# Kernel optimization log

Hardware: AMD Instinct MI355X
Metric: run time of the kernel (lower is better)

The kernel has to match this reference:

```python
import jax, jax.numpy as jnp
from jax import lax
import numpy as np

B, T, NL = 512, 64, 32          # batch, timepoints per patient, n_labs
LAT, HID = 64, 128              # latent_dim, hidden_dim
SCALE, STEP, QPAD, TMAX = 365.0, 0.05, 2000, 2000


def setup_inputs() -> dict:
    key = jax.random.key(0)
    k = jax.random.split(key, 24)
    def rn(ki, shape, s=0.05):
        return jax.random.normal(ki, shape, jnp.float32) * s
    Din = 2 * NL + 1  # GRU input: labs, mask, dt
    return {
        "obs_vals": rn(k[0], (B, T, NL), 1.0),
        "age": jax.random.uniform(k[1], (B,), jnp.float32),
        "eps": rn(k[2], (B, LAT), 1.0),  # reparameterization noise (randn_like)
        "gru_Wih": rn(k[3], (Din, 3 * HID)), "gru_Whh": rn(k[4], (HID, 3 * HID)),
        "gru_bih": jnp.zeros((3 * HID,)), "gru_bhh": jnp.zeros((3 * HID,)),
        "Wmu": rn(k[5], (HID, LAT)), "bmu": jnp.zeros((LAT,)),
        "Wlv": rn(k[6], (HID, LAT)), "blv": jnp.zeros((LAT,)),
        "W1": rn(k[7], (LAT, HID)), "b1": jnp.zeros((HID,)),
        "W2": rn(k[8], (HID, HID)), "b2": jnp.zeros((HID,)),
        "W3": rn(k[9], (HID, LAT)), "b3": jnp.zeros((LAT,)),
        "Wo1": rn(k[10], (LAT, HID)), "bo1": jnp.zeros((HID,)),
        "Wo2": rn(k[11], (HID, NL)), "bo2": jnp.zeros((NL,)),
        "Ws1": rn(k[12], (LAT + 1, HID)), "bs1": jnp.zeros((HID,)),
        "Ws2": rn(k[13], (HID, 2)), "bs2": jnp.zeros((2,)),
        "obs_mask": jax.random.bernoulli(k[14], 0.7, (B, T, NL)),
        "timepoints": jnp.sort(jax.random.randint(k[15], (B, T), 0, TMAX), axis=1).astype(jnp.int32),
        "seq_lens": jax.random.randint(k[16], (B,), 1, T + 1).astype(jnp.int32),
    }


def reference(obs_vals, age, eps, gru_Wih, gru_Whh, gru_bih, gru_bhh,
              Wmu, bmu, Wlv, blv, W1, b1, W2, b2, W3, b3,
              Wo1, bo1, Wo2, bo2, Ws1, bs1, Ws2, bs2,
              obs_mask, timepoints, seq_lens):
    Bv, Tv, Dv = obs_vals.shape
    Hdim = gru_Whh.shape[0]
    tp = timepoints.astype(jnp.float32)

    # ---- RecognitionRNN (GRU over reversed sequence) ----
    dt = jnp.concatenate([jnp.zeros((Bv, 1)), tp[:, 1:] - tp[:, :-1]], axis=1)[..., None]
    maskf = obs_mask.astype(obs_vals.dtype)
    inp = jnp.concatenate([obs_vals * maskf, maskf, dt], axis=-1)  # [B,T,2*NL+1]
    x_seq = jnp.flip(inp, axis=1).transpose(1, 0, 2)  # [T,B,Din]

    def gru_step(h, x):
        gi = x @ gru_Wih + gru_bih
        gh = h @ gru_Whh + gru_bhh
        ir, iz, i_n = jnp.split(gi, 3, axis=-1)
        hr, hz, hn = jnp.split(gh, 3, axis=-1)
        r = jax.nn.sigmoid(ir + hr)
        zg = jax.nn.sigmoid(iz + hz)
        n = jnp.tanh(i_n + r * hn)
        h = (1.0 - zg) * n + zg * h
        return h, None

    h, _ = lax.scan(gru_step, jnp.zeros((Bv, Hdim), obs_vals.dtype), x_seq)
    mu = h @ Wmu + bmu
    logvar = h @ Wlv + blv
    z0 = mu + eps * jnp.exp(0.5 * logvar)  # reparameterize

    # ---- query times (padded unique; timepoints are >= 0 by construction) ----
    qd = jnp.unique(timepoints.reshape(-1), size=QPAD, fill_value=timepoints.max())
    query_t = qd.astype(jnp.float32) / SCALE  # [Q], nondecreasing

    # ---- torchdiffeq fixed-grid rk4 with step_size ----
    qnp = np.asarray(query_t)
    t0, t1 = float(qnp[0]), float(qnp[-1])
    niters = int(np.ceil((t1 - t0) / STEP + 1))
    grid = np.arange(niters) * STEP + t0
    if grid[-1] > t1:
        grid[-1] = t1
    grid = jnp.asarray(grid, jnp.float32)  # [G]

    def ode_f(z):
        return jnp.tanh(jnp.tanh(z @ W1 + b1) @ W2 + b2) @ W3 + b3

    def rk4_step(y, hstep):
        k1 = ode_f(y)
        k2 = ode_f(y + 0.5 * hstep * k1)
        k3 = ode_f(y + 0.5 * hstep * k2)
        k4 = ode_f(y + hstep * k3)
        y2 = y + (hstep / 6.0) * (k1 + 2.0 * k2 + 2.0 * k3 + k4)
        return y2, y2

    _, ys = lax.scan(rk4_step, z0, grid[1:] - grid[:-1])
    ys = jnp.concatenate([z0[None], ys], axis=0)  # [G,B,L]

    # linear interpolation of grid states at query_t (torchdiffeq behavior)
    gi = jnp.clip(jnp.searchsorted(grid, query_t, side="right") - 1, 0, grid.shape[0] - 2)
    tl, tr = grid[gi], grid[gi + 1]
    w = ((query_t - tl) / jnp.where(tr - tl == 0, 1.0, tr - tl))[:, None, None]
    z_traj = ys[gi] * (1.0 - w) + ys[gi + 1] * w  # [Q,B,L]

    # ---- reconstruction loss (vectorized over B,T) ----
    tq = tp / SCALE  # [B,T]
    idx_q = jnp.argmin(jnp.abs(query_t[None, None, :] - tq[:, :, None]), axis=-1)  # [B,T]
    z_bt = z_traj[idx_q, jnp.arange(Bv)[:, None]]  # [B,T,L]
    x_hat = jax.nn.relu(z_bt @ Wo1 + bo1) @ Wo2 + bo2  # [B,T,NL]
    valid = (jnp.arange(Tv)[None, :] < seq_lens[:, None]).astype(obs_vals.dtype)[..., None]
    m = maskf * valid
    n_obs = m.sum()
    recon = jnp.where(n_obs > 0,
                      (m * (x_hat - obs_vals) ** 2).sum() / jnp.maximum(n_obs, 1.0),
                      0.0)

    kl = -0.5 * jnp.mean(jnp.sum(1.0 + logvar - mu ** 2 - jnp.exp(logvar), axis=-1))

    # ---- z_eval at last observed timepoint per patient ----
    last_tp = jnp.take_along_axis(tp, (seq_lens - 1)[:, None], axis=1)[:, 0] / SCALE  # [B]
    idx_e = jnp.argmin(jnp.abs(query_t[None, :] - last_tp[:, None]), axis=-1)  # [B]
    z_eval = z_traj[idx_e, jnp.arange(Bv)]  # [B,L]
    log_hazard = jax.nn.relu(jnp.concatenate([z_eval, age[:, None]], axis=-1) @ Ws1 + bs1) @ Ws2 + bs2
    return log_hazard, recon, kl, z_eval
```

## Files before the change

kernel.cpp:

```cpp
#include <hip/hip_runtime.h>
#include <hip/hip_bf16.h>
#include <math.h>

#define B 512
#define T 64
#define NL 32
#define LAT 64
#define HID 128
#define DIN 65
#define G3 384
#define FSCALE 365.0f
#define MAXGRID 128

#define WS_MIN   0
#define WS_MAX   1
#define WS_NIT   2
#define WS_KL    3
#define WS_RE    4
#define WS_NO    5
#define WS_GRID  8
#define WS_Z0    (WS_GRID + MAXGRID)
#define WS_YS    (WS_Z0 + B*LAT)
#define WS_W31   (WS_YS + 120*B*LAT)
#define WS_B31   (WS_W31 + HID*HID)

typedef __attribute__((ext_vector_type(8))) __bf16 bf16x8;
typedef __attribute__((ext_vector_type(4))) float f32x4;

static __device__ __forceinline__ float tanh_fast(float x){
    float t = __builtin_amdgcn_exp2f(x * 2.8853900817779268f);
    return 1.0f - 2.0f * __builtin_amdgcn_rcpf(t + 1.0f);
}
static __device__ __forceinline__ float sigmoid_fast(float x){
    return __builtin_amdgcn_rcpf(1.0f + __builtin_amdgcn_exp2f(-1.4426950408889634f * x));
}

__global__ void k_init(const int* __restrict__ tp, float* wsf){
    int* wsi = (int*)wsf;
    __shared__ int smin[256], smax[256];
    int tid = threadIdx.x;
    int mn = 2147483647, mx = -2147483647-1;
    for (int i = tid; i < B*T; i += 256){ int v = tp[i]; mn = min(mn,v); mx = max(mx,v); }
    smin[tid]=mn; smax[tid]=mx; __syncthreads();
    for (int s=128; s>0; s>>=1){
        if (tid<s){ smin[tid]=min(smin[tid],smin[tid+s]); smax[tid]=max(smax[tid],smax[tid+s]); }
        __syncthreads();
    }
    if (tid==0){
        wsi[WS_MIN]=smin[0]; wsi[WS_MAX]=smax[0];
        wsf[WS_KL]=0.f; wsf[WS_RE]=0.f; wsf[WS_NO]=0.f;
    }
}

__global__ void k_grid(float* wsf){
    int* wsi=(int*)wsf;
    float t0f = (float)wsi[WS_MIN] / FSCALE;
    float t1f = (float)wsi[WS_MAX] / FSCALE;
    double t0d = (double)t0f, t1d = (double)t1f;
    int nit = (int)ceil((t1d-t0d)/0.05 + 1.0);
    if (nit < 1) nit = 1;
    if (nit > MAXGRID) nit = MAXGRID;
    if (threadIdx.x==0) wsi[WS_NIT] = nit;
    int k = threadIdx.x;
    if (k < nit){
        double g = (double)k * 0.05 + t0d;
        if (k == nit-1 && g > t1d) g = t1d;
        wsf[WS_GRID + k] = (float)g;
    }
}

__global__ __launch_bounds__(256) void k_w31(
    const float* __restrict__ W1, const float* __restrict__ W3,
    const float* __restrict__ b3, float* wsf)
{
    int gid = blockIdx.x*256 + threadIdx.x;
    int k = gid >> 5, n0 = (gid & 31)*4;
    float4 acc = {0.f,0.f,0.f,0.f};
    #pragma unroll 8
    for (int l=0;l<64;++l){
        float w3v = W3[k*LAT + l];
        float4 w1v = *(const float4*)&W1[l*HID + n0];
        acc.x = fmaf(w3v, w1v.x, acc.x);
        acc.y = fmaf(w3v, w1v.y, acc.y);
        acc.z = fmaf(w3v, w1v.z, acc.z);
        acc.w = fmaf(w3v, w1v.w, acc.w);
    }
    *(float4*)&wsf[WS_W31 + k*HID + n0] = acc;
    if (blockIdx.x==0 && threadIdx.x < HID){
        int n = threadIdx.x; float a = 0.f;
        #pragma unroll 8
        for (int l=0;l<64;++l) a = fmaf(b3[l], W1[l*HID+n], a);
        wsf[WS_B31 + n] = a;
    }
}

__global__ __launch_bounds__(512) void k_gru(
    const float* __restrict__ obs, const float* __restrict__ eps,
    const float* __restrict__ Wih, const float* __restrict__ Whh,
    const float* __restrict__ bih, const float* __restrict__ bhh,
    const float* __restrict__ Wmu, const float* __restrict__ bmu,
    const float* __restrict__ Wlv, const float* __restrict__ blv,
    const int* __restrict__ maskI, const int* __restrict__ tp,
    float* wsf)
{
    const int b0 = blockIdx.x * 16;
    const int tid = threadIdx.x;
    const int w = tid >> 6, lane = tid & 63;
    const int g = lane >> 4, c = lane & 15;
    const int xr = tid >> 5, xl = tid & 31;

    __shared__ __align__(16) __bf16 xh[16][232];
    __shared__ int   tps[16][64];
    __shared__ float dts[16];
    __shared__ float lvs[16][64];
    __shared__ float red[8];

    ((int2*)tps)[tid] = ((const int2*)(tp + (size_t)b0*T))[tid];
    {
        unsigned* xz = (unsigned*)&xh[0][0];
        #pragma unroll
        for (int i=0;i<1856;i+=512) xz[i+tid] = 0u;
    }

    bf16x8 wr[6], wz[6], wi[2], wh[4];
    #pragma unroll
    for (int q=0;q<6;++q){
        int kt = q<2 ? q : q+1;
        #pragma unroll
        for (int e=0;e<8;++e){
            int k = kt*32 + g*8 + e;
            float vr, vz;
            if (k < 64){ vr = Wih[k*G3 + 16*w+c];      vz = Wih[k*G3 + 128+16*w+c]; }
            else       { vr = Whh[(k-96)*G3 + 16*w+c]; vz = Whh[(k-96)*G3 + 128+16*w+c]; }
            wr[q][e] = (__bf16)vr; wz[q][e] = (__bf16)vz;
        }
    }
    #pragma unroll
    for (int q=0;q<2;++q)
        #pragma unroll
        for (int e=0;e<8;++e)
            wi[q][e] = (__bf16)Wih[(q*32+g*8+e)*G3 + 256+16*w+c];
    #pragma unroll
    for (int q=0;q<4;++q)
        #pragma unroll
        for (int e=0;e<8;++e)
            wh[q][e] = (__bf16)Whh[(q*32+g*8+e)*G3 + 256+16*w+c];
    const float wdr = Wih[64*G3 + 16*w+c];
    const float wdz = Wih[64*G3 + 128+16*w+c];
    const float wdn = Wih[64*G3 + 256+16*w+c];
    const float rb  = bih[16*w+c]     + bhh[16*w+c];
    const float zb  = bih[128+16*w+c] + bhh[128+16*w+c];
    const float inb = bih[256+16*w+c];
    const float hnb = bhh[256+16*w+c];

    __syncthreads();

    {
        float mv = (float)maskI[((size_t)(b0+xr)*T + 63)*NL + xl];
        float ov = obs[((size_t)(b0+xr)*T + 63)*NL + xl];
        xh[xr][xl]    = (__bf16)(ov*mv);
        xh[xr][32+xl] = (__bf16)mv;
        if (xl==0) dts[xr] = (float)(tps[xr][63]-tps[xr][62]);
    }

    float hold[4] = {0.f,0.f,0.f,0.f};

    for (int s=0;s<T;++s){
        const int t = T-1-s;
        __syncthreads();
        bf16x8 A0 = *(const bf16x8*)&xh[c][0*32 + g*8];
        bf16x8 A1 = *(const bf16x8*)&xh[c][1*32 + g*8];
        bf16x8 A2 = *(const bf16x8*)&xh[c][3*32 + g*8];
        bf16x8 A3 = *(const bf16x8*)&xh[c][4*32 + g*8];
        bf16x8 A4 = *(const bf16x8*)&xh[c][5*32 + g*8];
        bf16x8 A5 = *(const bf16x8*)&xh[c][6*32 + g*8];
        const float dt0=dts[4*g], dt1=dts[4*g+1], dt2=dts[4*g+2], dt3=dts[4*g+3];
        float ov=0.f, mvn=0.f; const int tn = t-1;
        if (s < T-1){
            mvn = (float)maskI[((size_t)(b0+xr)*T + tn)*NL + xl];
            ov  = obs[((size_t)(b0+xr)*T + tn)*NL + xl];
        }
        f32x4 racc={0,0,0,0}, zacc={0,0,0,0}, inacc={0,0,0,0}, hnacc={0,0,0,0};
        racc  = __builtin_amdgcn_mfma_f32_16x16x32_bf16(A0, wr[0], racc, 0,0,0);
        zacc  = __builtin_amdgcn_mfma_f32_16x16x32_bf16(A0, wz[0], zacc, 0,0,0);
        inacc = __builtin_amdgcn_mfma_f32_16x16x32_bf16(A0, wi[0], inacc,0,0,0);
        hnacc = __builtin_amdgcn_mfma_f32_16x16x32_bf16(A2, wh[0], hnacc,0,0,0);
        racc  = __builtin_amdgcn_mfma_f32_16x16x32_bf16(A1, wr[1], racc, 0,0,0);
        zacc  = __builtin_amdgcn_mfma_f32_16x16x32_bf16(A1, wz[1], zacc, 0,0,0);
        inacc = __builtin_amdgcn_mfma_f32_16x16x32_bf16(A1, wi[1], inacc,0,0,0);
        hnacc = __builtin_amdgcn_mfma_f32_16x16x32_bf16(A3, wh[1], hnacc,0,0,0);
        racc  = __builtin_amdgcn_mfma_f32_16x16x32_bf16(A2, wr[2], racc, 0,0,0);
        zacc  = __builtin_amdgcn_mfma_f32_16x16x32_bf16(A2, wz[2], zacc, 0,0,0);
        hnacc = __builtin_amdgcn_mfma_f32_16x16x32_bf16(A4, wh[2], hnacc,0,0,0);
        racc  = __builtin_amdgcn_mfma_f32_16x16x32_bf16(A3, wr[3], racc, 0,0,0);
        zacc  = __builtin_amdgcn_mfma_f32_16x16x32_bf16(A3, wz[3], zacc, 0,0,0);
        hnacc = __builtin_amdgcn_mfma_f32_16x16x32_bf16(A5, wh[3], hnacc,0,0,0);
        racc  = __builtin_amdgcn_mfma_f32_16x16x32_bf16(A4, wr[4], racc, 0,0,0);
        zacc  = __builtin_amdgcn_mfma_f32_16x16x32_bf16(A4, wz[4], zacc, 0,0,0);
        racc  = __builtin_amdgcn_mfma_f32_16x16x32_bf16(A5, wr[5], racc, 0,0,0);
        zacc  = __builtin_amdgcn_mfma_f32_16x16x32_bf16(A5, wz[5], zacc, 0,0,0);
        float hnew[4]; const float dtv[4] = {dt0,dt1,dt2,dt3};
        #pragma unroll
        for (int j=0;j<4;++j){
            float dv = dtv[j];
            float r  = sigmoid_fast(racc[j] + rb + dv*wdr);
            float zg = sigmoid_fast(zacc[j] + zb + dv*wdz);
            float n  = tanh_fast(inacc[j] + inb + dv*wdn + r*(hnacc[j] + hnb));
            float hv = (1.f - zg)*n + zg*hold[j];
            hold[j] = hv; hnew[j] = hv;
        }
        __syncthreads();
        #pragma unroll
        for (int j=0;j<4;++j) xh[4*g+j][96+16*w+c] = (__bf16)hnew[j];
        if (s < T-1){
            xh[xr][xl]    = (__bf16)(ov*mvn);
            xh[xr][32+xl] = (__bf16)mvn;
            if (xl==0) dts[xr] = (tn>0) ? (float)(tps[xr][tn]-tps[xr][tn-1]) : 0.f;
        }
    }
    __syncthreads();

    const int col4 = 16*(w&3)+c;
    bf16x8 Ah0 = *(const bf16x8*)&xh[c][96+0*32+g*8];
    bf16x8 Ah1 = *(const bf16x8*)&xh[c][96+1*32+g*8];
    bf16x8 Ah2 = *(const bf16x8*)&xh[c][96+2*32+g*8];
    bf16x8 Ah3 = *(const bf16x8*)&xh[c][96+3*32+g*8];
    const float* Wm = (w<4)? Wmu : Wlv;
    f32x4 acc={0,0,0,0};
    {
        bf16x8 bf0,bf1,bf2,bf3;
        #pragma unroll
        for (int e=0;e<8;++e){
            bf0[e] = (__bf16)Wm[(0*32+g*8+e)*LAT + col4];
            bf1[e] = (__bf16)Wm[(1*32+g*8+e)*LAT + col4];
            bf2[e] = (__bf16)Wm[(2*32+g*8+e)*LAT + col4];
            bf3[e] = (__bf16)Wm[(3*32+g*8+e)*LAT + col4];
        }
        acc = __builtin_amdgcn_mfma_f32_16x16x32_bf16(Ah0, bf0, acc, 0,0,0);
        acc = __builtin_amdgcn_mfma_f32_16x16x32_bf16(Ah1, bf1, acc, 0,0,0);
        acc = __builtin_amdgcn_mfma_f32_16x16x32_bf16(Ah2, bf2, acc, 0,0,0);
        acc = __builtin_amdgcn_mfma_f32_16x16x32_bf16(Ah3, bf3, acc, 0,0,0);
    }
    const float mbias = (w<4)? bmu[col4] : blv[col4];
    if (w>=4){
        #pragma unroll
        for (int j=0;j<4;++j) lvs[4*g+j][col4] = acc[j] + mbias;
    }
    __syncthreads();
    if (w<4){
        float kl = 0.f;
        #pragma unroll
        for (int j=0;j<4;++j){
            float mu = acc[j] + mbias;
            float lv = lvs[4*g+j][col4];
            int row = b0 + 4*g + j;
            float z0 = mu + eps[(size_t)row*LAT + col4]*expf(0.5f*lv);
            wsf[WS_Z0 + (size_t)row*LAT + col4] = z0;
            wsf[WS_YS + (size_t)row*LAT + col4] = z0;
            kl += 1.f + lv - mu*mu - expf(lv);
        }
        #pragma unroll
        for (int off=32; off>0; off>>=1) kl += __shfl_xor(kl, off);
        if (lane==0) red[w] = kl;
    }
    __syncthreads();
    if (tid==0) atomicAdd(&wsf[WS_KL], red[0]+red[1]+red[2]+red[3]);
}

__global__ __launch_bounds__(256) void k_ode(
    const float* __restrict__ W1, const float* __restrict__ b1,
    const float* __restrict__ W2, const float* __restrict__ b2,
    const float* __restrict__ W3, const float* __restrict__ b3,
    float* wsf)
{
    const int b0 = blockIdx.x * 16;
    const int tid = threadIdx.x;
    const int w = tid >> 6, lane = tid & 63;
    const int g = lane >> 4, c = lane & 15;
    const int lc = 16*w + c;
    const int* wsi = (const int*)wsf;
    const int nit = wsi[WS_NIT];

    __shared__ __align__(16) __bf16 Gl[16][136];
    __shared__ __align__(16) __bf16 Hl[16][136];
    __shared__ float gls[MAXGRID];

    bf16x8 w2f[2][4], w31f[2][4], w3f[4];
    float b1v[2], b2v[2], b31v[2];
    #pragma unroll
    for (int t=0;t<2;++t){
        const int n = 32*w + 16*t + c;
        #pragma unroll
        for (int q=0;q<4;++q)
            #pragma unroll
            for (int e=0;e<8;++e){
                w2f[t][q][e]  = (__bf16)W2[(q*32+g*8+e)*HID + n];
                w31f[t][q][e] = (__bf16)wsf[WS_W31 + (q*32+g*8+e)*HID + n];
            }
        b1v[t]=b1[n]; b2v[t]=b2[n]; b31v[t]=wsf[WS_B31+n];
    }
    #pragma unroll
    for (int q=0;q<4;++q)
        #pragma unroll
        for (int e=0;e<8;++e)
            w3f[q][e] = (__bf16)W3[(q*32+g*8+e)*LAT + lc];
    const float b3v = b3[lc];

    for (int kk=tid; kk<MAXGRID; kk+=256) gls[kk]=wsf[WS_GRID+kk];

    {
        int r = tid>>4, l0 = (tid&15)*4;
        float4 zv = *(const float4*)&wsf[WS_Z0 + (size_t)(b0+r)*LAT + l0];
        Gl[r][l0]   = (__bf16)zv.x; Gl[r][l0+1] = (__bf16)zv.y;
        Gl[r][l0+2] = (__bf16)zv.z; Gl[r][l0+3] = (__bf16)zv.w;
    }
    float y[4];
    #pragma unroll
    for (int j=0;j<4;++j)
        y[j] = wsf[WS_Z0 + (size_t)(b0+4*g+j)*LAT + lc];
    __syncthreads();

    f32x4 U[2];
    {
        bf16x8 az0 = *(const bf16x8*)&Gl[c][g*8];
        bf16x8 az1 = *(const bf16x8*)&Gl[c][32+g*8];
        #pragma unroll
        for (int t=0;t<2;++t){
            const int n = 32*w + 16*t + c;
            bf16x8 wf0, wf1;
            #pragma unroll
            for (int e=0;e<8;++e){
                wf0[e] = (__bf16)W1[(g*8+e)*HID + n];
                wf1[e] = (__bf16)W1[(32+g*8+e)*HID + n];
            }
            f32x4 a = {0.f,0.f,0.f,0.f};
            a = __builtin_amdgcn_mfma_f32_16x16x32_bf16(az0, wf0, a, 0,0,0);
            a = __builtin_amdgcn_mfma_f32_16x16x32_bf16(az1, wf1, a, 0,0,0);
            U[t] = a;
        }
    }
    __syncthreads();

    #pragma unroll
    for (int t=0;t<2;++t)
        #pragma unroll
        for (int j=0;j<4;++j)
            Gl[4*g+j][32*w+16*t+c] = (__bf16)tanh_fast(U[t][j] + b1v[t]);
    __syncthreads();

    f32x4 Uacc0={0,0,0,0}, Uacc1={0,0,0,0}, faccv={0,0,0,0};

    for (int i=0; i<nit-1; ++i){
        const float h = gls[i+1]-gls[i];
        #pragma unroll
        for (int sub=0; sub<4; ++sub){
            {
                bf16x8 a0 = *(const bf16x8*)&Gl[c][g*8];
                bf16x8 a1 = *(const bf16x8*)&Gl[c][32+g*8];
                bf16x8 a2 = *(const bf16x8*)&Gl[c][64+g*8];
                bf16x8 a3 = *(const bf16x8*)&Gl[c][96+g*8];
                #pragma unroll
                for (int t=0;t<2;++t){
                    f32x4 ca={0,0,0,0}, cb={0,0,0,0};
                    ca = __builtin_amdgcn_mfma_f32_16x16x32_bf16(a0, w2f[t][0], ca, 0,0,0);
                    cb = __builtin_amdgcn_mfma_f32_16x16x32_bf16(a2, w2f[t][2], cb, 0,0,0);
                    ca = __builtin_amdgcn_mfma_f32_16x16x32_bf16(a1, w2f[t][1], ca, 0,0,0);
                    cb = __builtin_amdgcn_mfma_f32_16x16x32_bf16(a3, w2f[t][3], cb, 0,0,0);
                    #pragma unroll
                    for (int j=0;j<4;++j)
                        Hl[4*g+j][32*w+16*t+c] = (__bf16)tanh_fast(ca[j]+cb[j]+b2v[t]);
                }
            }
            __syncthreads();
            {
                bf16x8 h0 = *(const bf16x8*)&Hl[c][g*8];
                bf16x8 h1 = *(const bf16x8*)&Hl[c][32+g*8];
                bf16x8 h2 = *(const bf16x8*)&Hl[c][64+g*8];
                bf16x8 h3 = *(const bf16x8*)&Hl[c][96+g*8];
                f32x4 V[2];
                #pragma unroll
                for (int t=0;t<2;++t){
                    f32x4 ca={0,0,0,0}, cb={0,0,0,0};
                    ca = __builtin_amdgcn_mfma_f32_16x16x32_bf16(h0, w31f[t][0], ca, 0,0,0);
                    cb = __builtin_amdgcn_mfma_f32_16x16x32_bf16(h2, w31f[t][2], cb, 0,0,0);
                    ca = __builtin_amdgcn_mfma_f32_16x16x32_bf16(h1, w31f[t][1], ca, 0,0,0);
                    cb = __builtin_amdgcn_mfma_f32_16x16x32_bf16(h3, w31f[t][3], cb, 0,0,0);
                    #pragma unroll
                    for (int j=0;j<4;++j) V[t][j] = ca[j] + cb[j] + b31v[t];
                }
                f32x4 fa={0,0,0,0}, fb={0,0,0,0};
                fa = __builtin_amdgcn_mfma_f32_16x16x32_bf16(h0, w3f[0], fa, 0,0,0);
                fb = __builtin_amdgcn_mfma_f32_16x16x32_bf16(h2, w3f[2], fb, 0,0,0);
                fa = __builtin_amdgcn_mfma_f32_16x16x32_bf16(h1, w3f[1], fa, 0,0,0);
                fb = __builtin_amdgcn_mfma_f32_16x16x32_bf16(h3, w3f[3], fb, 0,0,0);
                if (sub==0){
                    #pragma unroll
                    for (int j=0;j<4;++j) faccv[j] = fa[j]+fb[j]+b3v;
                    Uacc0 = V[0]; Uacc1 = V[1];
                } else if (sub==3){
                    #pragma unroll
                    for (int j=0;j<4;++j) faccv[j] += fa[j]+fb[j]+b3v;
                    Uacc0 += V[0]; Uacc1 += V[1];
                } else {
                    #pragma unroll
                    for (int j=0;j<4;++j) faccv[j] += 2.f*(fa[j]+fb[j]+b3v);
                    Uacc0 += 2.f*V[0]; Uacc1 += 2.f*V[1];
                }
                if (sub < 3){
                    const float al = (sub==2) ? h : 0.5f*h;
                    #pragma unroll
                    for (int t=0;t<2;++t)
                        #pragma unroll
                        for (int j=0;j<4;++j)
                            Gl[4*g+j][32*w+16*t+c] =
                                (__bf16)tanh_fast(U[t][j] + al*V[t][j] + b1v[t]);
                } else {
                    const float h6 = h*(1.0f/6.0f);
                    #pragma unroll
                    for (int j=0;j<4;++j){
                        y[j] = fmaf(h6, faccv[j], y[j]);
                        wsf[WS_YS + ((size_t)(i+1)*B + (b0+4*g+j))*LAT + lc] = y[j];
                    }
                    U[0] += h6*Uacc0; U[1] += h6*Uacc1;
                    #pragma unroll
                    for (int t=0;t<2;++t)
                        #pragma unroll
                        for (int j=0;j<4;++j)
                            Gl[4*g+j][32*w+16*t+c] = (__bf16)tanh_fast(U[t][j] + b1v[t]);
                }
            }
            __syncthreads();
        }
    }
}

__global__ __launch_bounds__(512) void k_recon(
    const float* __restrict__ obs, const int* __restrict__ maskI,
    const int* __restrict__ tp, const int* __restrict__ seq,
    const float* __restrict__ Wo1, const float* __restrict__ bo1,
    const float* __restrict__ Wo2, const float* __restrict__ bo2,
    float* wsf)
{
    const int b = blockIdx.x, tid = threadIdx.x;
    const int w = tid >> 6, lane = tid & 63;
    const int g = lane >> 4, c = lane & 15;
    __shared__ __align__(16) __bf16 zbt[64][72];
    __shared__ __align__(16) __bf16 hb[64][136];
    __shared__ float gls[MAXGRID];
    __shared__ float red[16];
    const int* wsi=(const int*)wsf;
    const int nit = wsi[WS_NIT];
    for (int i=tid;i<MAXGRID;i+=512) gls[i]=wsf[WS_GRID+i];

    bf16x8 wo1f[2], wo2f[4];
    #pragma unroll
    for (int q=0;q<2;++q)
        #pragma unroll
        for (int e=0;e<8;++e)
            wo1f[q][e] = (__bf16)Wo1[(q*32+g*8+e)*HID + 16*w+c];
    {
        int n = w & 1;
        #pragma unroll
        for (int q=0;q<4;++q)
            #pragma unroll
            for (int e=0;e<8;++e)
                wo2f[q][e] = (__bf16)Wo2[(q*32+g*8+e)*NL + 16*n+c];
    }
    const float bo1v = bo1[16*w+c];
    const float bo2v = bo2[16*(w&1)+c];
    const int sl = seq[b];
    __syncthreads();

    {
        int t = tid >> 3, seg = tid & 7;
        float tq = (float)tp[b*T+t] / FSCALE;
        int lo=0, hi=nit;
        while (lo<hi){ int mid=(lo+hi)>>1; if (gls[mid]<=tq) lo=mid+1; else hi=mid; }
        int k = lo-1; if (k<0) k=0; if (nit>=2 && k>nit-2) k=nit-2; if (nit<2) k=0;
        float wq=0.f;
        if (nit>=2){ float tl=gls[k], tr=gls[k+1]; float den=(tr-tl==0.f)?1.f:(tr-tl); wq=(tq-tl)/den; }
        size_t o0 = (size_t)WS_YS + ((size_t)k*B + b)*LAT + seg*8;
        float4 za0 = *(const float4*)&wsf[o0];
        float4 za1 = *(const float4*)&wsf[o0+4];
        float4 zb0, zb1;
        if (nit>=2){
            zb0 = *(const float4*)&wsf[o0 + (size_t)B*LAT];
            zb1 = *(const float4*)&wsf[o0 + (size_t)B*LAT + 4];
        } else { zb0 = za0; zb1 = za1; }
        __bf16* dst = &zbt[t][seg*8];
        dst[0] = (__bf16)(za0.x*(1.f-wq)+zb0.x*wq);
        dst[1] = (__bf16)(za0.y*(1.f-wq)+zb0.y*wq);
        dst[2] = (__bf16)(za0.z*(1.f-wq)+zb0.z*wq);
        dst[3] = (__bf16)(za0.w*(1.f-wq)+zb0.w*wq);
        dst[4] = (__bf16)(za1.x*(1.f-wq)+zb1.x*wq);
        dst[5] = (__bf16)(za1.y*(1.f-wq)+zb1.y*wq);
        dst[6] = (__bf16)(za1.z*(1.f-wq)+zb1.z*wq);
        dst[7] = (__bf16)(za1.w*(1.f-wq)+zb1.w*wq);
    }
    __syncthreads();

    #pragma unroll
    for (int m=0;m<4;++m){
        f32x4 acc = {0.f,0.f,0.f,0.f};
        bf16x8 a0 = *(const bf16x8*)&zbt[16*m+c][g*8];
        bf16x8 a1 = *(const bf16x8*)&zbt[16*m+c][32+g*8];
        acc = __builtin_amdgcn_mfma_f32_16x16x32_bf16(a0, wo1f[0], acc, 0,0,0);
        acc = __builtin_amdgcn_mfma_f32_16x16x32_bf16(a1, wo1f[1], acc, 0,0,0);
        #pragma unroll
        for (int j=0;j<4;++j)
            hb[16*m+4*g+j][16*w+c] = (__bf16)fmaxf(acc[j] + bo1v, 0.f);
    }
    __syncthreads();

    float esum = 0.f, ncnt = 0.f;
    {
        int m = w >> 1, n = w & 1;
        f32x4 ca = {0.f,0.f,0.f,0.f}, cb = {0.f,0.f,0.f,0.f};
        bf16x8 a0 = *(const bf16x8*)&hb[16*m+c][g*8];
        bf16x8 a1 = *(const bf16x8*)&hb[16*m+c][32+g*8];
        bf16x8 a2 = *(const bf16x8*)&hb[16*m+c][64+g*8];
        bf16x8 a3 = *(const bf16x8*)&hb[16*m+c][96+g*8];
        ca = __builtin_amdgcn_mfma_f32_16x16x32_bf16(a0, wo2f[0], ca, 0,0,0);
        cb = __builtin_amdgcn_mfma_f32_16x16x32_bf16(a2, wo2f[2], cb, 0,0,0);
        ca = __builtin_amdgcn_mfma_f32_16x16x32_bf16(a1, wo2f[1], ca, 0,0,0);
        cb = __builtin_amdgcn_mfma_f32_16x16x32_bf16(a3, wo2f[3], cb, 0,0,0);
        #pragma unroll
        for (int j=0;j<4;++j){
            int t = 16*m + 4*g + j;
            int col = 16*n + c;
            float xh2 = (ca[j]+cb[j]) + bo2v;
            float mv = (float)maskI[(b*T+t)*NL+col] * ((t<sl)?1.f:0.f);
            float d = xh2 - obs[(b*T+t)*NL+col];
            esum = fmaf(mv*d, d, esum);
            ncnt += mv;
        }
    }
    #pragma unroll
    for (int off=32; off>0; off>>=1){
        esum += __shfl_xor(esum, off);
        ncnt += __shfl_xor(ncnt, off);
    }
    if (lane==0){ red[w] = esum; red[8+w] = ncnt; }
    __syncthreads();
    if (tid==0){
        float s=0.f, nn=0.f;
        #pragma unroll
        for (int i=0;i<8;++i){ s += red[i]; nn += red[8+i]; }
        atomicAdd(&wsf[WS_RE], s);
        atomicAdd(&wsf[WS_NO], nn);
    }
}

__global__ __launch_bounds__(128) void k_surv(
    const float* __restrict__ age, const int* __restrict__ tp, const int* __restrict__ seq,
    const float* __restrict__ Ws1, const float* __restrict__ bs1,
    const float* __restrict__ Ws2, const float* __restrict__ bs2,
    float* wsf, float* out)
{
    int b=blockIdx.x, tid=threadIdx.x;
    __shared__ float gls[MAXGRID];
    __shared__ float ze[64];
    __shared__ float pred[4];
    const int* wsi=(const int*)wsf; int nit=wsi[WS_NIT];
    for (int i=tid;i<MAXGRID;i+=128) gls[i]=wsf[WS_GRID+i];
    __syncthreads();
    int sl = seq[b];
    float tq = (float)tp[b*T + sl-1] / FSCALE;
    int lo=0,hi=nit;
    while(lo<hi){int mid=(lo+hi)>>1; if (gls[mid]<=tq) lo=mid+1; else hi=mid;}
    int k=lo-1; if(k<0)k=0; if(nit>=2 && k>nit-2)k=nit-2; if (nit<2) k=0;
    float w=0.f;
    if (nit>=2){ float tl=gls[k],tr=gls[k+1]; float den=(tr-tl==0.f)?1.f:(tr-tl); w=(tq-tl)/den; }
    if (tid<LAT){
        size_t o0 = (size_t)WS_YS + ((size_t)k*B+b)*LAT+tid;
        float zl = wsf[o0]*(1.f-w) + ((nit>=2)? wsf[o0+(size_t)B*LAT]*w : 0.f);
        ze[tid]=zl;
        out[1026 + b*LAT + tid] = zl;
    }
    __syncthreads();
    float hj = bs1[tid];
    #pragma unroll 8
    for (int l=0;l<LAT;++l) hj = fmaf(ze[l], Ws1[l*HID+tid], hj);
    hj = fmaf(age[b], Ws1[LAT*HID+tid], hj);
    hj = fmaxf(hj,0.f);
    float p0 = hj*Ws2[tid*2+0], p1 = hj*Ws2[tid*2+1];
    #pragma unroll
    for (int off=32;off>0;off>>=1){ p0 += __shfl_down(p0,off); p1 += __shfl_down(p1,off); }
    int wv = tid>>6;
    if ((tid&63)==0){ pred[wv*2]=p0; pred[wv*2+1]=p1; }
    __syncthreads();
    if (tid==0){
        out[b*2+0] = bs2[0] + pred[0]+pred[2];
        out[b*2+1] = bs2[1] + pred[1]+pred[3];
    }
}

__global__ void k_fin(float* wsf, float* out){
    float n = wsf[WS_NO];
    out[1024] = (n>0.f) ? (wsf[WS_RE]/fmaxf(n,1.f)) : 0.f;
    out[1025] = -0.5f * (wsf[WS_KL] / (float)B);
}

extern "C" void kernel_launch(void* const* d_in, const int* in_sizes, int n_in,
                              void* d_out, int out_size, void* d_ws, size_t ws_size,
                              hipStream_t stream) {
    const float* obs   = (const float*)d_in[0];
    const float* age   = (const float*)d_in[1];
    const float* eps   = (const float*)d_in[2];
    const float* Wih   = (const float*)d_in[3];
    const float* Whh   = (const float*)d_in[4];
    const float* bih   = (const float*)d_in[5];
    const float* bhh   = (const float*)d_in[6];
    const float* Wmu   = (const float*)d_in[7];
    const float* bmu   = (const float*)d_in[8];
    const float* Wlv   = (const float*)d_in[9];
    const float* blv   = (const float*)d_in[10];
    const float* W1    = (const float*)d_in[11];
    const float* b1    = (const float*)d_in[12];
    const float* W2    = (const float*)d_in[13];
    const float* b2    = (const float*)d_in[14];
    const float* W3    = (const float*)d_in[15];
    const float* b3    = (const float*)d_in[16];
    const float* Wo1   = (const float*)d_in[17];
    const float* bo1   = (const float*)d_in[18];
    const float* Wo2   = (const float*)d_in[19];
    const float* bo2   = (const float*)d_in[20];
    const float* Ws1   = (const float*)d_in[21];
    const float* bs1   = (const float*)d_in[22];
    const float* Ws2   = (const float*)d_in[23];
    const float* bs2   = (const float*)d_in[24];
    const int*   maskI = (const int*)d_in[25];
    const int*   tp    = (const int*)d_in[26];
    const int*   seq   = (const int*)d_in[27];
    float* wsf = (float*)d_ws;
    float* out = (float*)d_out;

    k_init<<<1, 256, 0, stream>>>(tp, wsf);
    k_grid<<<1, 128, 0, stream>>>(wsf);
    k_w31<<<16, 256, 0, stream>>>(W1, W3, b3, wsf);
    k_gru<<<B/16, 512, 0, stream>>>(obs, eps, Wih, Whh, bih, bhh, Wmu, bmu, Wlv, blv,
                                    maskI, tp, wsf);
    k_ode<<<B/16, 256, 0, stream>>>(W1, b1, W2, b2, W3, b3, wsf);
    k_recon<<<B, 512, 0, stream>>>(obs, maskI, tp, seq, Wo1, bo1, Wo2, bo2, wsf);
    k_surv<<<B, 128, 0, stream>>>(age, tp, seq, Ws1, bs1, Ws2, bs2, wsf, out);
    k_fin<<<1, 1, 0, stream>>>(wsf, out);
}
```

Baseline: 585.5 us.

## Split ODE kernel hidden columns across 8 waves instead of 4

The RK4 ODE kernel now launches 512 threads per block, so each wave owns one 16-column hidden tile instead of two. This halves the per-wave MFMA chain and tanh work on the sequential critical path. The W3/y output work is restricted to the first four waves. The cost is more waves taking part in each barrier, and idle waves during the W3 step.

New measurement: 528.6 us. 9.7% less time.

```diff
diff --git a/kernel.cpp b/kernel.cpp
--- a/kernel.cpp
+++ b/kernel.cpp
@@ -267,7 +267,7 @@
     if (tid==0) atomicAdd(&wsf[WS_KL], red[0]+red[1]+red[2]+red[3]);
 }
 
-__global__ __launch_bounds__(256) void k_ode(
+__global__ __launch_bounds__(512) void k_ode(
     const float* __restrict__ W1, const float* __restrict__ b1,
     const float* __restrict__ W2, const float* __restrict__ b2,
     const float* __restrict__ W3, const float* __restrict__ b3,
@@ -277,7 +277,8 @@
     const int tid = threadIdx.x;
     const int w = tid >> 6, lane = tid & 63;
     const int g = lane >> 4, c = lane & 15;
-    const int lc = 16*w + c;
+    const int hc = 16*w + c;
+    const int lc = 16*(w&3) + c;
     const int* wsi = (const int*)wsf;
     const int nit = wsi[WS_NIT];
 
@@ -285,34 +286,27 @@
     __shared__ __align__(16) __bf16 Hl[16][136];
     __shared__ float gls[MAXGRID];
 
-    bf16x8 w2f[2][4], w31f[2][4], w3f[4];
-    float b1v[2], b2v[2], b31v[2];
-    #pragma unroll
-    for (int t=0;t<2;++t){
-        const int n = 32*w + 16*t + c;
-        #pragma unroll
-        for (int q=0;q<4;++q)
-            #pragma unroll
-            for (int e=0;e<8;++e){
-                w2f[t][q][e]  = (__bf16)W2[(q*32+g*8+e)*HID + n];
-                w31f[t][q][e] = (__bf16)wsf[WS_W31 + (q*32+g*8+e)*HID + n];
-            }
-        b1v[t]=b1[n]; b2v[t]=b2[n]; b31v[t]=wsf[WS_B31+n];
-    }
+    bf16x8 w2f[4], w31f[4], w3f[4];
     #pragma unroll
     for (int q=0;q<4;++q)
         #pragma unroll
-        for (int e=0;e<8;++e)
-            w3f[q][e] = (__bf16)W3[(q*32+g*8+e)*LAT + lc];
-    const float b3v = b3[lc];
-
-    for (int kk=tid; kk<MAXGRID; kk+=256) gls[kk]=wsf[WS_GRID+kk];
-
-    {
-        int r = tid>>4, l0 = (tid&15)*4;
-        float4 zv = *(const float4*)&wsf[WS_Z0 + (size_t)(b0+r)*LAT + l0];
-        Gl[r][l0]   = (__bf16)zv.x; Gl[r][l0+1] = (__bf16)zv.y;
-        Gl[r][l0+2] = (__bf16)zv.z; Gl[r][l0+3] = (__bf16)zv.w;
+        for (int e=0;e<8;++e){
+            w2f[q][e]  = (__bf16)W2[(q*32+g*8+e)*HID + hc];
+            w31f[q][e] = (__bf16)wsf[WS_W31 + (q*32+g*8+e)*HID + hc];
+            w3f[q][e]  = (__bf16)W3[(q*32+g*8+e)*LAT + lc];
+        }
+    const float b1v  = b1[hc];
+    const float b2v  = b2[hc];
+    const float b31v = wsf[WS_B31 + hc];
+    const float b3v  = b3[lc];
+
+    for (int kk=tid; kk<MAXGRID; kk+=512) gls[kk]=wsf[WS_GRID+kk];
+
+    {
+        int r = tid >> 5, l0 = (tid & 31)*2;
+        float2 zv = *(const float2*)&wsf[WS_Z0 + (size_t)(b0+r)*LAT + l0];
+        Gl[r][l0]   = (__bf16)zv.x;
+        Gl[r][l0+1] = (__bf16)zv.y;
     }
     float y[4];
     #pragma unroll
@@ -320,35 +314,29 @@
         y[j] = wsf[WS_Z0 + (size_t)(b0+4*g+j)*LAT + lc];
     __syncthreads();
 
-    f32x4 U[2];
+    f32x4 U;
     {
         bf16x8 az0 = *(const bf16x8*)&Gl[c][g*8];
         bf16x8 az1 = *(const bf16x8*)&Gl[c][32+g*8];
-        #pragma unroll
-        for (int t=0;t<2;++t){
-            const int n = 32*w + 16*t + c;
-            bf16x8 wf0, wf1;
-            #pragma unroll
-            for (int e=0;e<8;++e){
-                wf0[e] = (__bf16)W1[(g*8+e)*HID + n];
-                wf1[e] = (__bf16)W1[(32+g*8+e)*HID + n];
-            }
-            f32x4 a = {0.f,0.f,0.f,0.f};
-            a = __builtin_amdgcn_mfma_f32_16x16x32_bf16(az0, wf0, a, 0,0,0);
-            a = __builtin_amdgcn_mfma_f32_16x16x32_bf16(az1, wf1, a, 0,0,0);
-            U[t] = a;
-        }
-    }
-    __syncthreads();
-
-    #pragma unroll
-    for (int t=0;t<2;++t)
-        #pragma unroll
-        for (int j=0;j<4;++j)
-            Gl[4*g+j][32*w+16*t+c] = (__bf16)tanh_fast(U[t][j] + b1v[t]);
-    __syncthreads();
-
-    f32x4 Uacc0={0,0,0,0}, Uacc1={0,0,0,0}, faccv={0,0,0,0};
+        bf16x8 wf0, wf1;
+        #pragma unroll
+        for (int e=0;e<8;++e){
+            wf0[e] = (__bf16)W1[(g*8+e)*HID + hc];
+            wf1[e] = (__bf16)W1[(32+g*8+e)*HID + hc];
+        }
+        f32x4 a = {0.f,0.f,0.f,0.f};
+        a = __builtin_amdgcn_mfma_f32_16x16x32_bf16(az0, wf0, a, 0,0,0);
+        a = __builtin_amdgcn_mfma_f32_16x16x32_bf16(az1, wf1, a, 0,0,0);
+        U = a;
+    }
+    __syncthreads();
+
+    #pragma unroll
+    for (int j=0;j<4;++j)
+        Gl[4*g+j][hc] = (__bf16)tanh_fast(U[j] + b1v);
+    __syncthreads();
+
+    f32x4 Uacc={0,0,0,0}, faccv={0,0,0,0};
 
     for (int i=0; i<nit-1; ++i){
         const float h = gls[i+1]-gls[i];
@@ -359,17 +347,14 @@
                 bf16x8 a1 = *(const bf16x8*)&Gl[c][32+g*8];
                 bf16x8 a2 = *(const bf16x8*)&Gl[c][64+g*8];
                 bf16x8 a3 = *(const bf16x8*)&Gl[c][96+g*8];
+                f32x4 ca={0,0,0,0}, cb={0,0,0,0};
+                ca = __builtin_amdgcn_mfma_f32_16x16x32_bf16(a0, w2f[0], ca, 0,0,0);
+                cb = __builtin_amdgcn_mfma_f32_16x16x32_bf16(a2, w2f[2], cb, 0,0,0);
+                ca = __builtin_amdgcn_mfma_f32_16x16x32_bf16(a1, w2f[1], ca, 0,0,0);
+                cb = __builtin_amdgcn_mfma_f32_16x16x32_bf16(a3, w2f[3], cb, 0,0,0);
                 #pragma unroll
-                for (int t=0;t<2;++t){
-                    f32x4 ca={0,0,0,0}, cb={0,0,0,0};
-                    ca = __builtin_amdgcn_mfma_f32_16x16x32_bf16(a0, w2f[t][0], ca, 0,0,0);
-                    cb = __builtin_amdgcn_mfma_f32_16x16x32_bf16(a2, w2f[t][2], cb, 0,0,0);
-                    ca = __builtin_amdgcn_mfma_f32_16x16x32_bf16(a1, w2f[t][1], ca, 0,0,0);
-                    cb = __builtin_amdgcn_mfma_f32_16x16x32_bf16(a3, w2f[t][3], cb, 0,0,0);
-                    #pragma unroll
-                    for (int j=0;j<4;++j)
-                        Hl[4*g+j][32*w+16*t+c] = (__bf16)tanh_fast(ca[j]+cb[j]+b2v[t]);
-                }
+                for (int j=0;j<4;++j)
+                    Hl[4*g+j][hc] = (__bf16)tanh_fast(ca[j]+cb[j]+b2v);
             }
             __syncthreads();
             {
@@ -377,56 +362,48 @@
                 bf16x8 h1 = *(const bf16x8*)&Hl[c][32+g*8];
                 bf16x8 h2 = *(const bf16x8*)&Hl[c][64+g*8];
                 bf16x8 h3 = *(const bf16x8*)&Hl[c][96+g*8];
-                f32x4 V[2];
+                f32x4 va={0,0,0,0}, vb={0,0,0,0};
+                va = __builtin_amdgcn_mfma_f32_16x16x32_bf16(h0, w31f[0], va, 0,0,0);
+                vb = __builtin_amdgcn_mfma_f32_16x16x32_bf16(h2, w31f[2], vb, 0,0,0);
+                va = __builtin_amdgcn_mfma_f32_16x16x32_bf16(h1, w31f[1], va, 0,0,0);
+                vb = __builtin_amdgcn_mfma_f32_16x16x32_bf16(h3, w31f[3], vb, 0,0,0);
+                f32x4 V;
                 #pragma unroll
-                for (int t=0;t<2;++t){
-                    f32x4 ca={0,0,0,0}, cb={0,0,0,0};
-                    ca = __builtin_amdgcn_mfma_f32_16x16x32_bf16(h0, w31f[t][0], ca, 0,0,0);
-                    cb = __builtin_amdgcn_mfma_f32_16x16x32_bf16(h2, w31f[t][2], cb, 0,0,0);
-                    ca = __builtin_amdgcn_mfma_f32_16x16x32_bf16(h1, w31f[t][1], ca, 0,0,0);
-                    cb = __builtin_amdgcn_mfma_f32_16x16x32_bf16(h3, w31f[t][3], cb, 0,0,0);
+                for (int j=0;j<4;++j) V[j] = va[j] + vb[j] + b31v;
+
+                f32x4 fv = {0,0,0,0};
+                if (w < 4){
+                    f32x4 fa={0,0,0,0}, fb={0,0,0,0};
+                    fa = __builtin_amdgcn_mfma_f32_16x16x32_bf16(h0, w3f[0], fa, 0,0,0);
+                    fb = __builtin_amdgcn_mfma_f32_16x16x32_bf16(h2, w3f[2], fb, 0,0,0);
+                    fa = __builtin_amdgcn_mfma_f32_16x16x32_bf16(h1, w3f[1], fa, 0,0,0);
+                    fb = __builtin_amdgcn_mfma_f32_16x16x32_bf16(h3, w3f[3], fb, 0,0,0);
                     #pragma unroll
-                    for (int j=0;j<4;++j) V[t][j] = ca[j] + cb[j] + b31v[t];
+                    for (int j=0;j<4;++j) fv[j] = fa[j] + fb[j] + b3v;
                 }
-                f32x4 fa={0,0,0,0}, fb={0,0,0,0};
-                fa = __builtin_amdgcn_mfma_f32_16x16x32_bf16(h0, w3f[0], fa, 0,0,0);
-                fb = __builtin_amdgcn_mfma_f32_16x16x32_bf16(h2, w3f[2], fb, 0,0,0);
-                fa = __builtin_amdgcn_mfma_f32_16x16x32_bf16(h1, w3f[1], fa, 0,0,0);
-                fb = __builtin_amdgcn_mfma_f32_16x16x32_bf16(h3, w3f[3], fb, 0,0,0);
-                if (sub==0){
-                    #pragma unroll
-                    for (int j=0;j<4;++j) faccv[j] = fa[j]+fb[j]+b3v;
-                    Uacc0 = V[0]; Uacc1 = V[1];
-                } else if (sub==3){
-                    #pragma unroll
-                    for (int j=0;j<4;++j) faccv[j] += fa[j]+fb[j]+b3v;
-                    Uacc0 += V[0]; Uacc1 += V[1];
-                } else {
-                    #pragma unroll
-                    for (int j=0;j<4;++j) faccv[j] += 2.f*(fa[j]+fb[j]+b3v);
-                    Uacc0 += 2.f*V[0]; Uacc1 += 2.f*V[1];
-                }
+                if (sub==0){ Uacc = V; faccv = fv; }
+                else if (sub==3){ Uacc += V; faccv += fv; }
+                else { Uacc += 2.f*V; faccv += 2.f*fv; }
+
                 if (sub < 3){
                     const float al = (sub==2) ? h : 0.5f*h;
                     #pragma unroll
-                    for (int t=0;t<2;++t)
-                        #pragma unroll
-                        for (int j=0;j<4;++j)
-                            Gl[4*g+j][32*w+16*t+c] =
-                                (__bf16)tanh_fast(U[t][j] + al*V[t][j] + b1v[t]);
+                    for (int j=0;j<4;++j)
+                        Gl[4*g+j][hc] = (__bf16)tanh_fast(fmaf(al, V[j], U[j]) + b1v);
                 } else {
                     const float h6 = h*(1.0f/6.0f);
+                    if (w < 4){
+                        #pragma unroll
+                        for (int j=0;j<4;++j){
+                            y[j] = fmaf(h6, faccv[j], y[j]);
+                            wsf[WS_YS + ((size_t)(i+1)*B + (b0+4*g+j))*LAT + lc] = y[j];
+                        }
+                    }
                     #pragma unroll
                     for (int j=0;j<4;++j){
-                        y[j] = fmaf(h6, faccv[j], y[j]);
-                        wsf[WS_YS + ((size_t)(i+1)*B + (b0+4*g+j))*LAT + lc] = y[j];
+                        U[j] = fmaf(h6, Uacc[j], U[j]);
+                        Gl[4*g+j][hc] = (__bf16)tanh_fast(U[j] + b1v);
                     }
-                    U[0] += h6*Uacc0; U[1] += h6*Uacc1;
-                    #pragma unroll
-                    for (int t=0;t<2;++t)
-                        #pragma unroll
-                        for (int j=0;j<4;++j)
-                            Gl[4*g+j][32*w+16*t+c] = (__bf16)tanh_fast(U[t][j] + b1v[t]);
                 }
             }
             __syncthreads();
@@ -640,7 +617,7 @@
     k_w31<<<16, 256, 0, stream>>>(W1, W3, b3, wsf);
     k_gru<<<B/16, 512, 0, stream>>>(obs, eps, Wih, Whh, bih, bhh, Wmu, bmu, Wlv, blv,
                                     maskI, tp, wsf);
-    k_ode<<<B/16, 256, 0, stream>>>(W1, b1, W2, b2, W3, b3, wsf);
+    k_ode<<<B/16, 512, 0, stream>>>(W1, b1, W2, b2, W3, b3, wsf);
     k_recon<<<B, 512, 0, stream>>>(obs, maskI, tp, seq, Wo1, bo1, Wo2, bo2, wsf);
     k_surv<<<B, 128, 0, stream>>>(age, tp, seq, Ws1, bs1, Ws2, bs2, wsf, out);
     k_fin<<<1, 1, 0, stream>>>(wsf, out);
```
